# Performance work log

Hardware: AMD Instinct MI355X
Metric: run time of the kernel (lower is better)

The kernel has to match this reference:

```python
import jax, jax.numpy as jnp
import numpy as np

T, IN_DIM, H1, H2 = 64, 84, 128, 84
BATCH = 8192


def _glorot(key, shape, fan):
    bound = 1.0 / np.sqrt(fan)
    return jax.random.uniform(key, shape, jnp.float32, -bound, bound)


def setup_inputs() -> dict:
    key = jax.random.key(0)
    ks = jax.random.split(key, 13)
    x = jax.random.normal(ks[0], (BATCH, T, IN_DIM, 1), jnp.float32)
    # rnn1 layer 0: 84 -> 128
    w_ih_l0 = _glorot(ks[1], (H1, IN_DIM), H1)
    w_hh_l0 = _glorot(ks[2], (H1, H1), H1)
    b_ih_l0 = _glorot(ks[3], (H1,), H1)
    b_hh_l0 = _glorot(ks[4], (H1,), H1)
    # rnn1 layer 1: 128 -> 128
    w_ih_l1 = _glorot(ks[5], (H1, H1), H1)
    w_hh_l1 = _glorot(ks[6], (H1, H1), H1)
    b_ih_l1 = _glorot(ks[7], (H1,), H1)
    b_hh_l1 = _glorot(ks[8], (H1,), H1)
    # rnn2: 128 -> 84
    w_ih_l2 = _glorot(ks[9], (H2, H1), H2)
    w_hh_l2 = _glorot(ks[10], (H2, H2), H2)
    b_ih_l2 = _glorot(ks[11], (H2,), H2)
    b_hh_l2 = _glorot(ks[12], (H2,), H2)
    return {
        "x": x,
        "w_ih_l0": w_ih_l0, "w_hh_l0": w_hh_l0, "b_ih_l0": b_ih_l0, "b_hh_l0": b_hh_l0,
        "w_ih_l1": w_ih_l1, "w_hh_l1": w_hh_l1, "b_ih_l1": b_ih_l1, "b_hh_l1": b_hh_l1,
        "w_ih_l2": w_ih_l2, "w_hh_l2": w_hh_l2, "b_ih_l2": b_ih_l2, "b_hh_l2": b_hh_l2,
    }


def _elman_layer(x, w_ih, w_hh, b_ih, b_hh):
    # x: (B, T, I) -> (B, T, H); h_t = tanh(x_t W_ih^T + b_ih + h_{t-1} W_hh^T + b_hh)
    # Precompute the input projection for all timesteps as one big GEMM.
    xp = jnp.einsum('bti,hi->bth', x, w_ih) + (b_ih + b_hh)  # (B, T, H)
    h0 = jnp.zeros((x.shape[0], w_hh.shape[0]), x.dtype)

    def step(h, xp_t):
        h = jnp.tanh(xp_t + h @ w_hh.T)
        return h, h

    _, ys = jax.lax.scan(step, h0, jnp.swapaxes(xp, 0, 1))  # (T, B, H)
    return jnp.swapaxes(ys, 0, 1)


def reference(x,
              w_ih_l0, w_hh_l0, b_ih_l0, b_hh_l0,
              w_ih_l1, w_hh_l1, b_ih_l1, b_hh_l1,
              w_ih_l2, w_hh_l2, b_ih_l2, b_hh_l2):
    x_ = jnp.squeeze(x, -1)                                   # (B, 64, 84)
    h = _elman_layer(x_, w_ih_l0, w_hh_l0, b_ih_l0, b_hh_l0)  # (B, 64, 128)
    h = _elman_layer(h, w_ih_l1, w_hh_l1, b_ih_l1, b_hh_l1)   # (B, 64, 128)
    h = _elman_layer(h, w_ih_l2, w_hh_l2, b_ih_l2, b_hh_l2)   # (B, 64, 84)
    return h[..., None]                                       # (B, 64, 84, 1)
```

## Files before the change

### kernel.cpp

```cpp
#include <hip/hip_runtime.h>


typedef __bf16 bf16x8 __attribute__((ext_vector_type(8)));
typedef float  f32x4  __attribute__((ext_vector_type(4)));
typedef float  f32x16 __attribute__((ext_vector_type(16)));
typedef unsigned short u16;
typedef unsigned int   u32;
typedef u16 u16x8 __attribute__((ext_vector_type(8)));
typedef u16 u16x4 __attribute__((ext_vector_type(4)));

#define MFMA32(a, b, c) __builtin_amdgcn_mfma_f32_32x32x16_bf16((a), (b), (c), 0, 0, 0)

__device__ __forceinline__ float bf2f(u16 v) {
    return __builtin_bit_cast(float, (u32)v << 16);
}
__device__ __forceinline__ u16 f2bf(float f) {
    u32 u = __builtin_bit_cast(u32, f);
    u = u + 0x7fffu + ((u >> 16) & 1u);
    return (u16)(u >> 16);
}
__device__ __forceinline__ float tanh_fast(float x) {
    float xc = fminf(fmaxf(x, -12.f), 12.f);
    float e  = __expf(2.f * xc);
    return (e - 1.f) * __builtin_amdgcn_rcpf(e + 1.f);
}
__device__ __forceinline__ bf16x8 ld_lds8(const u16* p) {
    return __builtin_bit_cast(bf16x8, *(const u16x8*)p);
}
__device__ __forceinline__ int aswz(int row, int off) {
    return row * 128 + (off ^ ((row & 7) << 3));
}
__device__ __forceinline__ void store4_hl(u16* ph, u16* pl, f32x4 v) {
    u16x4 hi, lo;
#pragma unroll
    for (int j = 0; j < 4; j++) {
        u16 h = f2bf(v[j]);
        hi[j] = h;
        lo[j] = f2bf(v[j] - bf2f(h));
    }
    *(u16x4*)ph = hi;
    *(u16x4*)pl = lo;
}

struct fragp { bf16x8 h, l; };

__device__ __forceinline__ fragp load_wfrag_hl(const float* W, int Hr, int Kr,
                                               int n, int kbase) {
    u16x8 uh = {0,0,0,0,0,0,0,0}, ul = {0,0,0,0,0,0,0,0};
    if (n < Hr) {
#pragma unroll
        for (int j = 0; j < 8; j++) {
            int k = kbase + j;
            if (k < Kr) {
                float w = W[n * Kr + k];
                u16 hi = f2bf(w);
                uh[j] = hi;
                ul[j] = f2bf(w - bf2f(hi));
            }
        }
    }
    fragp r;
    r.h = __builtin_bit_cast(bf16x8, uh);
    r.l = __builtin_bit_cast(bf16x8, ul);
    return r;
}

__device__ __forceinline__ f32x16 mm3t(const fragp& w, bf16x8 ah, bf16x8 al, f32x16 c) {
    c = MFMA32(w.h, ah, c);
    c = MFMA32(w.l, ah, c);
    c = MFMA32(w.h, al, c);
    return c;
}

#define STG_ISSUE(trr)                                                   \
    {                                                                    \
        const int tofs = (trr) * 84;                                     \
        xq0 = *(const f32x4*)&xg[goffq0 + tofs];                         \
        if (tid_s < 160) xq1 = *(const f32x4*)&xg[goffq1 + tofs];        \
    }
#define STG_WRITE(PNv)                                                   \
    {                                                                    \
        u16* bh = &xbh[(PNv)][0];                                        \
        u16* bl = &xbl[(PNv)][0];                                        \
        store4_hl(&bh[lofsq0], &bl[lofsq0], xq0);                        \
        if (tid_s < 160) store4_hl(&bh[lofsq1], &bl[lofsq1], xq1);       \
    }
#define STG_SETUP()                                                      \
    int goffq0, lofsq0, goffq1, lofsq1;                                  \
    {                                                                    \
        int r0 = tid_s / 21, c0 = (tid_s - r0 * 21) * 4;                 \
        goffq0 = r0 * 5376 + c0;                                         \
        lofsq0 = r0 * 128 + (c0 ^ ((r0 & 7) << 3));                      \
        int s1 = tid_s + 512, r1 = s1 / 21, c1 = (s1 - r1 * 21) * 4;     \
        goffq1 = r1 * 5376 + c1;                                         \
        lofsq1 = r1 * 128 + (c1 ^ ((r1 & 7) << 3));                      \
    }                                                                    \
    f32x4 xq0, xq1;

__global__ __launch_bounds__(768, 3)
void rnn_fused(const float* __restrict__ x,
               const float* __restrict__ wih0, const float* __restrict__ whh0,
               const float* __restrict__ bih0, const float* __restrict__ bhh0,
               const float* __restrict__ wih1, const float* __restrict__ whh1,
               const float* __restrict__ bih1, const float* __restrict__ bhh1,
               const float* __restrict__ wih2, const float* __restrict__ whh2,
               const float* __restrict__ bih2, const float* __restrict__ bhh2,
               float* __restrict__ out)
{
    __shared__ __align__(16) u16 h0h[2][4096], h0l[2][4096];
    __shared__ __align__(16) u16 h1h[2][4096], h1l[2][4096];
    __shared__ __align__(16) u16 h2h[2][4096], h2l[2][4096];
    __shared__ __align__(16) u16 xbh[2][4096], xbl[2][4096];
    __shared__ float biasF[3][128];

    const int tid  = threadIdx.x;
    const int wv   = tid >> 6;
    const int lane = tid & 63;
    const int mrow = lane & 31;
    const int q2   = lane >> 5;
    const int kq   = q2 * 8;
    const int q4   = q2 * 4;
    const int b0   = blockIdx.x * 32;
    const float* xg = x + (long)b0 * 5376;

    { u16* z = &h0h[0][0]; for (int i = tid; i < 4096; i += 768) z[i] = 0; }
    { u16* z = &h0l[0][0]; for (int i = tid; i < 4096; i += 768) z[i] = 0; }
    { u16* z = &h1h[1][0]; for (int i = tid; i < 4096; i += 768) z[i] = 0; }
    { u16* z = &h1l[1][0]; for (int i = tid; i < 4096; i += 768) z[i] = 0; }
    { u16* z = &h2h[0][0]; for (int i = tid; i < 4096; i += 768) z[i] = 0; }
    { u16* z = &h2l[0][0]; for (int i = tid; i < 4096; i += 768) z[i] = 0; }
    { u16* z = &xbh[0][0]; for (int i = tid; i < 8192; i += 768) z[i] = 0; }
    { u16* z = &xbl[0][0]; for (int i = tid; i < 8192; i += 768) z[i] = 0; }
    for (int s = tid; s < 672; s += 768) {
        int row = s / 21, cq = (s - row * 21) * 4;
        f32x4 v = *(const f32x4*)&xg[(long)row * 5376 + cq];
        int idx = row * 128 + (cq ^ ((row & 7) << 3));
        store4_hl(&xbh[0][idx], &xbl[0][idx], v);
    }
    for (int i = tid; i < 384; i += 768) {
        int l = i >> 7, n = i & 127;
        float v = 0.f;
        if (l == 0)      v = bih0[n] + bhh0[n];
        else if (l == 1) v = bih1[n] + bhh1[n];
        else if (n < 84) v = bih2[n] + bhh2[n];
        biasF[l][n] = v;
    }
    __syncthreads();

    if (wv < 4) {
        const int nb = wv * 32;
        fragp fih0[6], fhh0[8];
#pragma unroll
        for (int c = 0; c < 6; c++)
            fih0[c] = load_wfrag_hl(wih0, 128, 84, nb + mrow, c * 16 + kq);
#pragma unroll
        for (int c = 0; c < 8; c++)
            fhh0[c] = load_wfrag_hl(whh0, 128, 128, nb + mrow, c * 16 + kq);
        const int tid_s = wv * 64 + lane;
        STG_SETUP();

        for (int rr = 0; rr < 66; ++rr) {
            const int P = rr & 1, PN = P ^ 1;
            if (rr <= 62) STG_ISSUE(rr + 1);
            if (rr <= 63) {
                f32x16 accA, accB;
#pragma unroll
                for (int g = 0; g < 4; g++) {
                    f32x4 v = *(const f32x4*)&biasF[0][nb + g * 8 + q4];
                    accA[4*g+0] = v[0]; accA[4*g+1] = v[1];
                    accA[4*g+2] = v[2]; accA[4*g+3] = v[3];
                }
#pragma unroll
                for (int i = 0; i < 16; i++) accB[i] = 0.f;
                __builtin_amdgcn_s_setprio(1);
#pragma unroll
                for (int c = 0; c < 6; c++) {
                    const int idx = aswz(mrow, c * 16 + kq);
                    bf16x8 ah = ld_lds8(&xbh[P][idx]), al = ld_lds8(&xbl[P][idx]);
                    if (c & 1) accA = mm3t(fih0[c], ah, al, accA);
                    else       accB = mm3t(fih0[c], ah, al, accB);
                }
#pragma unroll
                for (int c = 0; c < 8; c++) {
                    const int idx = aswz(mrow, c * 16 + kq);
                    bf16x8 ah = ld_lds8(&h0h[P][idx]), al = ld_lds8(&h0l[P][idx]);
                    if (c & 1) accA = mm3t(fhh0[c], ah, al, accA);
                    else       accB = mm3t(fhh0[c], ah, al, accB);
                }
                __builtin_amdgcn_s_setprio(0);
                f32x16 acc = accA + accB;
#pragma unroll
                for (int g = 0; g < 4; g++) {
                    const int col = nb + g * 8 + q4;
                    f32x4 v;
                    v[0] = tanh_fast(acc[4*g+0]); v[1] = tanh_fast(acc[4*g+1]);
                    v[2] = tanh_fast(acc[4*g+2]); v[3] = tanh_fast(acc[4*g+3]);
                    const int idx = mrow * 128 + (col ^ ((mrow & 7) << 3));
                    store4_hl(&h0h[PN][idx], &h0l[PN][idx], v);
                }
            }
            if (rr <= 62) STG_WRITE(PN);
            __syncthreads();
        }
    } else if (wv < 8) {
        const int nb = (wv - 4) * 32;
        fragp fih1[8], fhh1[8];
#pragma unroll
        for (int c = 0; c < 8; c++) {
            fih1[c] = load_wfrag_hl(wih1, 128, 128, nb + mrow, c * 16 + kq);
            fhh1[c] = load_wfrag_hl(whh1, 128, 128, nb + mrow, c * 16 + kq);
        }
        for (int rr = 0; rr < 66; ++rr) {
            const int P = rr & 1, PN = P ^ 1;
            if (rr >= 1 && rr <= 64) {
                f32x16 accA, accB;
#pragma unroll
                for (int g = 0; g < 4; g++) {
                    f32x4 v = *(const f32x4*)&biasF[1][nb + g * 8 + q4];
                    accA[4*g+0] = v[0]; accA[4*g+1] = v[1];
                    accA[4*g+2] = v[2]; accA[4*g+3] = v[3];
                }
#pragma unroll
                for (int i = 0; i < 16; i++) accB[i] = 0.f;
                __builtin_amdgcn_s_setprio(1);
#pragma unroll
                for (int c = 0; c < 8; c++) {
                    const int idx = aswz(mrow, c * 16 + kq);
                    bf16x8 ah = ld_lds8(&h0h[P][idx]), al = ld_lds8(&h0l[P][idx]);
                    if (c & 1) accA = mm3t(fih1[c], ah, al, accA);
                    else       accB = mm3t(fih1[c], ah, al, accB);
                }
#pragma unroll
                for (int c = 0; c < 8; c++) {
                    const int idx = aswz(mrow, c * 16 + kq);
                    bf16x8 ah = ld_lds8(&h1h[P][idx]), al = ld_lds8(&h1l[P][idx]);
                    if (c & 1) accA = mm3t(fhh1[c], ah, al, accA);
                    else       accB = mm3t(fhh1[c], ah, al, accB);
                }
                __builtin_amdgcn_s_setprio(0);
                f32x16 acc = accA + accB;
#pragma unroll
                for (int g = 0; g < 4; g++) {
                    const int col = nb + g * 8 + q4;
                    f32x4 v;
                    v[0] = tanh_fast(acc[4*g+0]); v[1] = tanh_fast(acc[4*g+1]);
                    v[2] = tanh_fast(acc[4*g+2]); v[3] = tanh_fast(acc[4*g+3]);
                    const int idx = mrow * 128 + (col ^ ((mrow & 7) << 3));
                    store4_hl(&h1h[PN][idx], &h1l[PN][idx], v);
                }
            }
            __syncthreads();
        }
    } else if (wv < 11) {
        const int nb = (wv - 8) * 32;
        fragp fih2[8], fhh2[6];
#pragma unroll
        for (int c = 0; c < 8; c++)
            fih2[c] = load_wfrag_hl(wih2, 84, 128, nb + mrow, c * 16 + kq);
#pragma unroll
        for (int c = 0; c < 6; c++)
            fhh2[c] = load_wfrag_hl(whh2, 84, 84, nb + mrow, c * 16 + kq);
        const int tid_s = (wv - 4) * 64 + lane;
        STG_SETUP();

        for (int rr = 0; rr < 66; ++rr) {
            const int P = rr & 1, PN = P ^ 1;
            if (rr <= 62) STG_ISSUE(rr + 1);
            if (rr >= 2) {
                const int t2 = rr - 2;
                f32x16 accA, accB;
#pragma unroll
                for (int g = 0; g < 4; g++) {
                    f32x4 v = *(const f32x4*)&biasF[2][nb + g * 8 + q4];
                    accA[4*g+0] = v[0]; accA[4*g+1] = v[1];
                    accA[4*g+2] = v[2]; accA[4*g+3] = v[3];
                }
#pragma unroll
                for (int i = 0; i < 16; i++) accB[i] = 0.f;
                __builtin_amdgcn_s_setprio(1);
#pragma unroll
                for (int c = 0; c < 8; c++) {
                    const int idx = aswz(mrow, c * 16 + kq);
                    bf16x8 ah = ld_lds8(&h1h[P][idx]), al = ld_lds8(&h1l[P][idx]);
                    if (c & 1) accA = mm3t(fih2[c], ah, al, accA);
                    else       accB = mm3t(fih2[c], ah, al, accB);
                }
#pragma unroll
                for (int c = 0; c < 6; c++) {
                    const int idx = aswz(mrow, c * 16 + kq);
                    bf16x8 ah = ld_lds8(&h2h[P][idx]), al = ld_lds8(&h2l[P][idx]);
                    if (c & 1) accA = mm3t(fhh2[c], ah, al, accA);
                    else       accB = mm3t(fhh2[c], ah, al, accB);
                }
                __builtin_amdgcn_s_setprio(0);
                f32x16 acc = accA + accB;
#pragma unroll
                for (int g = 0; g < 4; g++) {
                    const int col = nb + g * 8 + q4;
                    f32x4 v;
                    v[0] = tanh_fast(acc[4*g+0]); v[1] = tanh_fast(acc[4*g+1]);
                    v[2] = tanh_fast(acc[4*g+2]); v[3] = tanh_fast(acc[4*g+3]);
                    const int idx = mrow * 128 + (col ^ ((mrow & 7) << 3));
                    store4_hl(&h2h[PN][idx], &h2l[PN][idx], v);
                    if (col < 84)
                        *(f32x4*)(out + (long)(b0 + mrow) * 5376 + t2 * 84 + col) = v;
                }
            }
            if (rr <= 62) STG_WRITE(PN);
            __syncthreads();
        }
    } else {
        const int tid_s = 7 * 64 + lane;
        STG_SETUP();
        for (int rr = 0; rr < 66; ++rr) {
            const int PN = (rr & 1) ^ 1;
            if (rr <= 62) STG_ISSUE(rr + 1);
            if (rr <= 62) STG_WRITE(PN);
            __syncthreads();
        }
    }
}

extern "C" void kernel_launch(void* const* d_in, const int* in_sizes, int n_in,
                              void* d_out, int out_size, void* d_ws, size_t ws_size,
                              hipStream_t stream) {
    (void)in_sizes; (void)n_in; (void)out_size; (void)d_ws; (void)ws_size;
    const float* x    = (const float*)d_in[0];
    const float* wih0 = (const float*)d_in[1];
    const float* whh0 = (const float*)d_in[2];
    const float* bih0 = (const float*)d_in[3];
    const float* bhh0 = (const float*)d_in[4];
    const float* wih1 = (const float*)d_in[5];
    const float* whh1 = (const float*)d_in[6];
    const float* bih1 = (const float*)d_in[7];
    const float* bhh1 = (const float*)d_in[8];
    const float* wih2 = (const float*)d_in[9];
    const float* whh2 = (const float*)d_in[10];
    const float* bih2 = (const float*)d_in[11];
    const float* bhh2 = (const float*)d_in[12];
    float* out = (float*)d_out;

    rnn_fused<<<dim3(8192 / 32), dim3(768), 0, stream>>>(
        x, wih0, whh0, bih0, bhh0, wih1, whh1, bih1, bhh1,
        wih2, whh2, bih2, bhh2, out);
}
```

Before: 592.6 us.

## Simplify tanh, use hardware bf16 conversion, single accumulator, lighter round barrier

Rewrites tanh as 1 - 2/(e+1) to drop a subtract and multiply. Replaces the manual round-to-nearest bf16 conversion with the native __bf16 cast, which can lower to hardware convert instructions. Merges the two interleaved MFMA accumulators into one chain, which removes the final vector add but serialises the MFMA dependency chain. Replaces __syncthreads with a barrier that waits only on LDS counters, so outstanding global loads can stay in flight across rounds. It also adds an extra sync after zeroing.

```diff
diff --git a/kernel.cpp b/kernel.cpp
--- a/kernel.cpp
+++ b/kernel.cpp
@@ -22,7 +22,8 @@
 __device__ __forceinline__ float tanh_fast(float x) {
     float xc = fminf(fmaxf(x, -12.f), 12.f);
     float e  = __expf(2.f * xc);
-    return (e - 1.f) * __builtin_amdgcn_rcpf(e + 1.f);
+    float r  = __builtin_amdgcn_rcpf(e + 1.f);
+    return __builtin_fmaf(-2.f, r, 1.f);
 }
 __device__ __forceinline__ bf16x8 ld_lds8(const u16* p) {
     return __builtin_bit_cast(bf16x8, *(const u16x8*)p);
@@ -34,9 +35,10 @@
     u16x4 hi, lo;
 #pragma unroll
     for (int j = 0; j < 4; j++) {
-        u16 h = f2bf(v[j]);
-        hi[j] = h;
-        lo[j] = f2bf(v[j] - bf2f(h));
+        __bf16 h = (__bf16)v[j];
+        hi[j] = __builtin_bit_cast(u16, h);
+        __bf16 l = (__bf16)(v[j] - bf2f(hi[j]));
+        lo[j] = __builtin_bit_cast(u16, l);
     }
     *(u16x4*)ph = hi;
     *(u16x4*)pl = lo;
@@ -71,6 +73,13 @@
     c = MFMA32(w.h, al, c);
     return c;
 }
+
+#define ROUND_BARRIER() do {                                             \
+    asm volatile("s_waitcnt lgkmcnt(0)" ::: "memory");                   \
+    __builtin_amdgcn_sched_barrier(0);                                   \
+    __builtin_amdgcn_s_barrier();                                        \
+    __builtin_amdgcn_sched_barrier(0);                                   \
+} while (0)
 
 #define STG_ISSUE(trr)                                                   \
     {                                                                    \
@@ -131,6 +140,7 @@
     { u16* z = &h2l[0][0]; for (int i = tid; i < 4096; i += 768) z[i] = 0; }
     { u16* z = &xbh[0][0]; for (int i = tid; i < 8192; i += 768) z[i] = 0; }
     { u16* z = &xbl[0][0]; for (int i = tid; i < 8192; i += 768) z[i] = 0; }
+    __syncthreads();
     for (int s = tid; s < 672; s += 768) {
         int row = s / 21, cq = (s - row * 21) * 4;
         f32x4 v = *(const f32x4*)&xg[(long)row * 5376 + cq];
@@ -163,32 +173,25 @@
             const int P = rr & 1, PN = P ^ 1;
             if (rr <= 62) STG_ISSUE(rr + 1);
             if (rr <= 63) {
-                f32x16 accA, accB;
+                f32x16 acc;
 #pragma unroll
                 for (int g = 0; g < 4; g++) {
                     f32x4 v = *(const f32x4*)&biasF[0][nb + g * 8 + q4];
-                    accA[4*g+0] = v[0]; accA[4*g+1] = v[1];
-                    accA[4*g+2] = v[2]; accA[4*g+3] = v[3];
-                }
-#pragma unroll
-                for (int i = 0; i < 16; i++) accB[i] = 0.f;
+                    acc[4*g+0] = v[0]; acc[4*g+1] = v[1];
+                    acc[4*g+2] = v[2]; acc[4*g+3] = v[3];
+                }
                 __builtin_amdgcn_s_setprio(1);
 #pragma unroll
                 for (int c = 0; c < 6; c++) {
                     const int idx = aswz(mrow, c * 16 + kq);
-                    bf16x8 ah = ld_lds8(&xbh[P][idx]), al = ld_lds8(&xbl[P][idx]);
-                    if (c & 1) accA = mm3t(fih0[c], ah, al, accA);
-                    else       accB = mm3t(fih0[c], ah, al, accB);
+                    acc = mm3t(fih0[c], ld_lds8(&xbh[P][idx]), ld_lds8(&xbl[P][idx]), acc);
                 }
 #pragma unroll
                 for (int c = 0; c < 8; c++) {
                     const int idx = aswz(mrow, c * 16 + kq);
-                    bf16x8 ah = ld_lds8(&h0h[P][idx]), al = ld_lds8(&h0l[P][idx]);
-                    if (c & 1) accA = mm3t(fhh0[c], ah, al, accA);
-                    else       accB = mm3t(fhh0[c], ah, al, accB);
+                    acc = mm3t(fhh0[c], ld_lds8(&h0h[P][idx]), ld_lds8(&h0l[P][idx]), acc);
                 }
                 __builtin_amdgcn_s_setprio(0);
-                f32x16 acc = accA + accB;
 #pragma unroll
                 for (int g = 0; g < 4; g++) {
                     const int col = nb + g * 8 + q4;
@@ -200,7 +203,7 @@
                 }
             }
             if (rr <= 62) STG_WRITE(PN);
-            __syncthreads();
+            ROUND_BARRIER();
         }
     } else if (wv < 8) {
         const int nb = (wv - 4) * 32;
@@ -213,32 +216,25 @@
         for (int rr = 0; rr < 66; ++rr) {
             const int P = rr & 1, PN = P ^ 1;
             if (rr >= 1 && rr <= 64) {
-                f32x16 accA, accB;
+                f32x16 acc;
 #pragma unroll
                 for (int g = 0; g < 4; g++) {
                     f32x4 v = *(const f32x4*)&biasF[1][nb + g * 8 + q4];
-                    accA[4*g+0] = v[0]; accA[4*g+1] = v[1];
-                    accA[4*g+2] = v[2]; accA[4*g+3] = v[3];
-                }
-#pragma unroll
-                for (int i = 0; i < 16; i++) accB[i] = 0.f;
+                    acc[4*g+0] = v[0]; acc[4*g+1] = v[1];
+                    acc[4*g+2] = v[2]; acc[4*g+3] = v[3];
+                }
                 __builtin_amdgcn_s_setprio(1);
 #pragma unroll
                 for (int c = 0; c < 8; c++) {
                     const int idx = aswz(mrow, c * 16 + kq);
-                    bf16x8 ah = ld_lds8(&h0h[P][idx]), al = ld_lds8(&h0l[P][idx]);
-                    if (c & 1) accA = mm3t(fih1[c], ah, al, accA);
-                    else       accB = mm3t(fih1[c], ah, al, accB);
+                    acc = mm3t(fih1[c], ld_lds8(&h0h[P][idx]), ld_lds8(&h0l[P][idx]), acc);
                 }
 #pragma unroll
                 for (int c = 0; c < 8; c++) {
                     const int idx = aswz(mrow, c * 16 + kq);
-                    bf16x8 ah = ld_lds8(&h1h[P][idx]), al = ld_lds8(&h1l[P][idx]);
-                    if (c & 1) accA = mm3t(fhh1[c], ah, al, accA);
-                    else       accB = mm3t(fhh1[c], ah, al, accB);
+                    acc = mm3t(fhh1[c], ld_lds8(&h1h[P][idx]), ld_lds8(&h1l[P][idx]), acc);
                 }
                 __builtin_amdgcn_s_setprio(0);
-                f32x16 acc = accA + accB;
 #pragma unroll
                 for (int g = 0; g < 4; g++) {
                     const int col = nb + g * 8 + q4;
@@ -249,7 +245,7 @@
                     store4_hl(&h1h[PN][idx], &h1l[PN][idx], v);
                 }
             }
-            __syncthreads();
+            ROUND_BARRIER();
         }
     } else if (wv < 11) {
         const int nb = (wv - 8) * 32;
@@ -268,32 +264,25 @@
             if (rr <= 62) STG_ISSUE(rr + 1);
             if (rr >= 2) {
                 const int t2 = rr - 2;
-                f32x16 accA, accB;
+                f32x16 acc;
 #pragma unroll
                 for (int g = 0; g < 4; g++) {
                     f32x4 v = *(const f32x4*)&biasF[2][nb + g * 8 + q4];
-                    accA[4*g+0] = v[0]; accA[4*g+1] = v[1];
-                    accA[4*g+2] = v[2]; accA[4*g+3] = v[3];
-                }
-#pragma unroll
-                for (int i = 0; i < 16; i++) accB[i] = 0.f;
+                    acc[4*g+0] = v[0]; acc[4*g+1] = v[1];
+                    acc[4*g+2] = v[2]; acc[4*g+3] = v[3];
+                }
                 __builtin_amdgcn_s_setprio(1);
 #pragma unroll
                 for (int c = 0; c < 8; c++) {
                     const int idx = aswz(mrow, c * 16 + kq);
-                    bf16x8 ah = ld_lds8(&h1h[P][idx]), al = ld_lds8(&h1l[P][idx]);
-                    if (c & 1) accA = mm3t(fih2[c], ah, al, accA);
-                    else       accB = mm3t(fih2[c], ah, al, accB);
+                    acc = mm3t(fih2[c], ld_lds8(&h1h[P][idx]), ld_lds8(&h1l[P][idx]), acc);
                 }
 #pragma unroll
                 for (int c = 0; c < 6; c++) {
                     const int idx = aswz(mrow, c * 16 + kq);
-                    bf16x8 ah = ld_lds8(&h2h[P][idx]), al = ld_lds8(&h2l[P][idx]);
-                    if (c & 1) accA = mm3t(fhh2[c], ah, al, accA);
-                    else       accB = mm3t(fhh2[c], ah, al, accB);
+                    acc = mm3t(fhh2[c], ld_lds8(&h2h[P][idx]), ld_lds8(&h2l[P][idx]), acc);
                 }
                 __builtin_amdgcn_s_setprio(0);
-                f32x16 acc = accA + accB;
 #pragma unroll
                 for (int g = 0; g < 4; g++) {
                     const int col = nb + g * 8 + q4;
@@ -307,7 +296,7 @@
                 }
             }
             if (rr <= 62) STG_WRITE(PN);
-            __syncthreads();
+            ROUND_BARRIER();
         }
     } else {
         const int tid_s = 7 * 64 + lane;
@@ -316,7 +305,7 @@
             const int PN = (rr & 1) ^ 1;
             if (rr <= 62) STG_ISSUE(rr + 1);
             if (rr <= 62) STG_WRITE(PN);
-            __syncthreads();
+            ROUND_BARRIER();
         }
     }
 }
```

Result: faster. 496.6 us (-16.2%).
